# Performance work log

Hardware: AMD Instinct MI355X
Metric: run time of the kernel (lower is better)

## Reference

```python
import jax, jax.numpy as jnp
import numpy as np

B, S1, S2, H1, H2, HID = 8, 512, 512, 128, 128, 128

def setup_inputs() -> dict:
    key = jax.random.key(0)
    ks = jax.random.split(key, 8)
    return {
        "query": jax.random.normal(ks[0], (B, S1, H1), jnp.float32),
        "key": jax.random.normal(ks[1], (B, S2, H2), jnp.float32),
        "value": jax.random.normal(ks[2], (B, S2, H2), jnp.float32),
        "q_mask": jax.random.randint(ks[3], (B, S1), 0, 2, jnp.int32),
        "k_mask": jax.random.randint(ks[4], (B, S2), 0, 2, jnp.int32),
        # init_weights: Linear weight ~ N(0, 0.01), bias = 0
        "W1": jax.random.normal(ks[5], (HID, H1 + H2), jnp.float32) * 0.01,
        "b1": jnp.zeros((HID,), jnp.float32),
        "W2": jax.random.normal(ks[6], (1, HID), jnp.float32) * 0.01,
        "b2": jnp.zeros((1,), jnp.float32),
    }

def reference(query, key, value, q_mask, k_mask, W1, b1, W2, b2):
    h1 = query.shape[-1]
    # Linear on concat([q,k]) == q @ W1[:, :h1].T + k @ W1[:, h1:].T + b1
    qp = jnp.einsum('bsd,hd->bsh', query, W1[:, :h1]) + b1   # [B,S1,HID]
    kp = jnp.einsum('btd,hd->bth', key, W1[:, h1:])          # [B,S2,HID]
    h = jax.nn.relu(qp[:, :, None, :] + kp[:, None, :, :])   # [B,S1,S2,HID]
    s = jnp.einsum('bsth,h->bst', h, W2[0]) + b2[0]          # [B,S1,S2]
    mask = (q_mask[:, :, None] * k_mask[:, None, :]) > 0     # [B,S1,S2]
    A = jnp.where(mask, jnp.exp(s), 0.0)                     # masked_fill(-inf).exp()
    A_sum = jnp.clip(jnp.sum(A, axis=-1, keepdims=True), 2e-15, None)
    attn = A / A_sum
    return jnp.einsum('bst,btd->bsd', attn, value)           # [B,S1,H2]
```

## Files before the change

### kernel.cpp

```cpp
#include <hip/hip_runtime.h>

#define S 512
#define H 128
#define NROW 4096
#define TI 8

__global__ __launch_bounds__(256) void w1t_kernel(const float* __restrict__ W1,
                                                  float* __restrict__ w1T) {
  __shared__ float t[32][33];
  const int d0 = (blockIdx.x & 7) * 32;
  const int h0 = (blockIdx.x >> 3) * 32;
  const int tx = threadIdx.x & 31, ty = threadIdx.x >> 5;
  #pragma unroll
  for (int r = 0; r < 4; r++)
    t[ty + r * 8][tx] = W1[(h0 + ty + r * 8) * 256 + d0 + tx];
  __syncthreads();
  #pragma unroll
  for (int r = 0; r < 4; r++)
    w1T[(size_t)(d0 + ty + r * 8) * H + h0 + tx] = t[tx][ty + r * 8];
}

__global__ __launch_bounds__(256) void proj_kernel(
    const float* __restrict__ query, const float* __restrict__ key,
    const float* __restrict__ w1T, const float* __restrict__ b1,
    const float* __restrict__ W2, const float* __restrict__ b2,
    float* __restrict__ qp, float* __restrict__ kp2,
    float* __restrict__ qw, float* __restrict__ kw)
{
  const int bid = blockIdx.x;
  const bool isq = bid < 256;
  const float* __restrict__ src = isq ? query : key;
  const int rbase = (isq ? bid : bid - 256) * 16;
  const int doff = isq ? 0 : 128;
  const int tid = threadIdx.x;
  const int w = __builtin_amdgcn_readfirstlane(tid >> 6);
  const int lane = tid & 63;
  const int r0w = rbase + w * 4;

  float acc[4][2];
  float2 bv = make_float2(0.f, 0.f);
  if (isq) bv = *(const float2*)(b1 + 2 * lane);
  #pragma unroll
  for (int r = 0; r < 4; r++) { acc[r][0] = bv.x; acc[r][1] = bv.y; }

  for (int dc = 0; dc < 128; dc += 8) {
    float qs[4][8];
    #pragma unroll
    for (int r = 0; r < 4; r++) {
      const float* sp = src + (size_t)(r0w + r) * H + dc;
      #pragma unroll
      for (int u = 0; u < 8; u++) qs[r][u] = sp[u];
    }
    #pragma unroll
    for (int dd = 0; dd < 8; dd++) {
      const float2 wv =
          *(const float2*)(w1T + (size_t)(doff + dc + dd) * H + 2 * lane);
      #pragma unroll
      for (int r = 0; r < 4; r++) {
        acc[r][0] = __builtin_fmaf(qs[r][dd], wv.x, acc[r][0]);
        acc[r][1] = __builtin_fmaf(qs[r][dd], wv.y, acc[r][1]);
      }
    }
  }

  const float2 w2p = *(const float2*)(W2 + 2 * lane);
  const float b2v = b2[0];
  #pragma unroll
  for (int r = 0; r < 4; r++) {
    float t = acc[r][0] * w2p.x + acc[r][1] * w2p.y;
    #pragma unroll
    for (int m = 1; m <= 32; m <<= 1) t += __shfl_xor(t, m, 64);
    if (lane == 0) {
      if (isq) qw[r0w + r] = 0.5f * t + b2v;
      else     kw[r0w + r] = 0.5f * t;
    }
  }

  if (isq) {
    #pragma unroll
    for (int r = 0; r < 4; r++)
      *(float2*)(qp + (size_t)(r0w + r) * H + 2 * lane) =
          make_float2(acc[r][0], acc[r][1]);
  } else {
    #pragma unroll
    for (int r = 0; r < 4; r++)
      *(float2*)(kp2 + ((size_t)(lane >> 3) * NROW + (r0w + r)) * 16 +
                 (lane & 7) * 2) = make_float2(acc[r][0], acc[r][1]);
  }
}

__global__ __launch_bounds__(512) void attn_kernel(
    const float* __restrict__ qp, const float* __restrict__ kp2,
    const float* __restrict__ qw, const float* __restrict__ kw,
    const float* __restrict__ value, const int* __restrict__ q_mask,
    const int* __restrict__ k_mask, const float* __restrict__ W2,
    float* __restrict__ out)
{
  __shared__ float aT[8][64][8];
  __shared__ float numw[8][TI][132];
  __shared__ float denw[8][TI];

  const int it = blockIdx.x;
  const int r0 = it * TI;
  const int b  = r0 >> 9;
  const int tid = threadIdx.x;
  const int w = __builtin_amdgcn_readfirstlane(tid >> 6);
  const int lane = tid & 63;
  const int jg = (b << 9) + (w << 6) + lane;
  const int km = k_mask[jg];
  const float kwj = kw[jg];

  float s[TI];
  #pragma unroll
  for (int i = 0; i < TI; i++) s[i] = 0.f;

  #pragma unroll
  for (int hb = 0; hb < 8; hb++) {
    const float* __restrict__ kptr = kp2 + (((size_t)hb * NROW + jg) << 4);
    const float4 k0 = ((const float4*)kptr)[0];
    const float4 k1 = ((const float4*)kptr)[1];
    const float4 k2 = ((const float4*)kptr)[2];
    const float4 k3 = ((const float4*)kptr)[3];
    const float4* __restrict__ w2c = (const float4*)(W2 + hb * 16);
    const float4 w0 = w2c[0], w1 = w2c[1], w2_ = w2c[2], w3 = w2c[3];
    #pragma unroll
    for (int i = 0; i < TI; i++) {
      const float4* __restrict__ qptr =
          (const float4*)(qp + (size_t)(r0 + i) * H + hb * 16);
      const float4 q0 = qptr[0], q1 = qptr[1], q2 = qptr[2], q3 = qptr[3];
      float t, si = s[i];
      t = q0.x + k0.x; si = __builtin_fmaf(fabsf(t), w0.x, si);
      t = q0.y + k0.y; si = __builtin_fmaf(fabsf(t), w0.y, si);
      t = q0.z + k0.z; si = __builtin_fmaf(fabsf(t), w0.z, si);
      t = q0.w + k0.w; si = __builtin_fmaf(fabsf(t), w0.w, si);
      t = q1.x + k1.x; si = __builtin_fmaf(fabsf(t), w1.x, si);
      t = q1.y + k1.y; si = __builtin_fmaf(fabsf(t), w1.y, si);
      t = q1.z + k1.z; si = __builtin_fmaf(fabsf(t), w1.z, si);
      t = q1.w + k1.w; si = __builtin_fmaf(fabsf(t), w1.w, si);
      t = q2.x + k2.x; si = __builtin_fmaf(fabsf(t), w2_.x, si);
      t = q2.y + k2.y; si = __builtin_fmaf(fabsf(t), w2_.y, si);
      t = q2.z + k2.z; si = __builtin_fmaf(fabsf(t), w2_.z, si);
      t = q2.w + k2.w; si = __builtin_fmaf(fabsf(t), w2_.w, si);
      t = q3.x + k3.x; si = __builtin_fmaf(fabsf(t), w3.x, si);
      t = q3.y + k3.y; si = __builtin_fmaf(fabsf(t), w3.y, si);
      t = q3.z + k3.z; si = __builtin_fmaf(fabsf(t), w3.z, si);
      t = q3.w + k3.w; si = __builtin_fmaf(fabsf(t), w3.w, si);
      s[i] = si;
    }
  }

  float a[TI];
  #pragma unroll
  for (int i = 0; i < TI; i++) {
    const float qws = qw[r0 + i];
    const int qm = q_mask[r0 + i];
    a[i] = (km > 0 && qm > 0) ? __expf(__builtin_fmaf(0.5f, s[i], qws + kwj))
                              : 0.f;
  }
  #pragma unroll
  for (int i = 0; i < TI; i += 2)
    *(float2*)&aT[w][lane][i] = make_float2(a[i], a[i + 1]);
  __syncthreads();

  const int lj = lane >> 5, lh = lane & 31;
  float nr[TI][4];
  float dden[TI];
  #pragma unroll
  for (int i = 0; i < TI; i++) {
    nr[i][0] = 0.f; nr[i][1] = 0.f; nr[i][2] = 0.f; nr[i][3] = 0.f;
    dden[i] = 0.f;
  }
  const float* __restrict__ vbase =
      value + ((size_t)b * S + (w << 6)) * H;

  for (int js = 0; js < 32; js++) {
    const int j = js * 2 + lj;
    const float4 vv = *(const float4*)(vbase + (size_t)j * H + lh * 4);
    const float4 a0 = *(const float4*)&aT[w][j][0];
    const float4 a1 = *(const float4*)&aT[w][j][4];
    const float av[8] = {a0.x, a0.y, a0.z, a0.w, a1.x, a1.y, a1.z, a1.w};
    #pragma unroll
    for (int i = 0; i < TI; i++) {
      nr[i][0] = __builtin_fmaf(av[i], vv.x, nr[i][0]);
      nr[i][1] = __builtin_fmaf(av[i], vv.y, nr[i][1]);
      nr[i][2] = __builtin_fmaf(av[i], vv.z, nr[i][2]);
      nr[i][3] = __builtin_fmaf(av[i], vv.w, nr[i][3]);
      dden[i] += av[i];
    }
  }
  #pragma unroll
  for (int i = 0; i < TI; i++) {
    #pragma unroll
    for (int k = 0; k < 4; k++) nr[i][k] += __shfl_xor(nr[i][k], 32, 64);
    dden[i] += __shfl_xor(dden[i], 32, 64);
  }
  if (lj == 0) {
    #pragma unroll
    for (int i = 0; i < TI; i++)
      *(float4*)&numw[w][i][lh * 4] =
          make_float4(nr[i][0], nr[i][1], nr[i][2], nr[i][3]);
    if (lane == 0) {
      #pragma unroll
      for (int i = 0; i < TI; i++) denw[w][i] = dden[i];
    }
  }
  __syncthreads();

  {
    const int i = w;
    float2 acc = make_float2(0.f, 0.f);
    float den = 0.f;
    #pragma unroll
    for (int ww = 0; ww < 8; ww++) {
      const float2 p = *(const float2*)&numw[ww][i][lane * 2];
      acc.x += p.x; acc.y += p.y;
      den += denw[ww][i];
    }
    const float inv = 1.f / fmaxf(den, 2e-15f);
    *(float2*)(out + (size_t)(r0 + i) * H + lane * 2) =
        make_float2(acc.x * inv, acc.y * inv);
  }
}

extern "C" void kernel_launch(void* const* d_in, const int* in_sizes, int n_in,
                              void* d_out, int out_size, void* d_ws, size_t ws_size,
                              hipStream_t stream)
{
  (void)in_sizes; (void)n_in; (void)out_size; (void)ws_size;
  const float* query  = (const float*)d_in[0];
  const float* key    = (const float*)d_in[1];
  const float* value  = (const float*)d_in[2];
  const int*   q_mask = (const int*)d_in[3];
  const int*   k_mask = (const int*)d_in[4];
  const float* W1     = (const float*)d_in[5];
  const float* b1     = (const float*)d_in[6];
  const float* W2     = (const float*)d_in[7];
  const float* b2     = (const float*)d_in[8];
  float* out = (float*)d_out;

  float* ws   = (float*)d_ws;
  float* w1T  = ws;
  float* qp   = w1T + 256 * H;
  float* kp2  = qp + (size_t)NROW * H;
  float* qw   = kp2 + (size_t)NROW * H;
  float* kw   = qw + NROW;

  w1t_kernel<<<32, 256, 0, stream>>>(W1, w1T);
  proj_kernel<<<512, 256, 0, stream>>>(query, key, w1T, b1, W2, b2,
                                       qp, kp2, qw, kw);
  attn_kernel<<<512, 512, 0, stream>>>(qp, kp2, qw, kw, value, q_mask,
                                       k_mask, W2, out);
}
```

Baseline: 128.6 us.

## Restructure score loop into row pairs with occupancy hint and drop redundant barrier

The attention score phase now walks four 32-wide hidden chunks, keeping key and W2 chunks in registers and processing query rows two at a time in non-unrolled loops. The kernel also gets a minimum-occupancy launch bound of 4 blocks. The barrier after writing the per-wave aT tile is removed, since each wave reads only its own slice. The projection kernel processes 16-wide chunks and preloads the W1 slices before the FMAs. Together these aim to cut register pressure and raise occupancy, at the risk of spills under the tighter register cap and less instruction-level parallelism from the rolled loops.

Measured after the change: 125.0 us. -2.8%, faster.

```diff
diff --git a/kernel.cpp b/kernel.cpp
--- a/kernel.cpp
+++ b/kernel.cpp
@@ -43,22 +43,25 @@
   #pragma unroll
   for (int r = 0; r < 4; r++) { acc[r][0] = bv.x; acc[r][1] = bv.y; }
 
-  for (int dc = 0; dc < 128; dc += 8) {
-    float qs[4][8];
+  #pragma unroll 1
+  for (int dc = 0; dc < 128; dc += 16) {
+    float qs[4][16];
     #pragma unroll
     for (int r = 0; r < 4; r++) {
       const float* sp = src + (size_t)(r0w + r) * H + dc;
       #pragma unroll
-      for (int u = 0; u < 8; u++) qs[r][u] = sp[u];
-    }
-    #pragma unroll
-    for (int dd = 0; dd < 8; dd++) {
-      const float2 wv =
-          *(const float2*)(w1T + (size_t)(doff + dc + dd) * H + 2 * lane);
+      for (int u = 0; u < 16; u++) qs[r][u] = sp[u];
+    }
+    float2 wv[16];
+    #pragma unroll
+    for (int dd = 0; dd < 16; dd++)
+      wv[dd] = *(const float2*)(w1T + (size_t)(doff + dc + dd) * H + 2 * lane);
+    #pragma unroll
+    for (int dd = 0; dd < 16; dd++) {
       #pragma unroll
       for (int r = 0; r < 4; r++) {
-        acc[r][0] = __builtin_fmaf(qs[r][dd], wv.x, acc[r][0]);
-        acc[r][1] = __builtin_fmaf(qs[r][dd], wv.y, acc[r][1]);
+        acc[r][0] = __builtin_fmaf(qs[r][dd], wv[dd].x, acc[r][0]);
+        acc[r][1] = __builtin_fmaf(qs[r][dd], wv[dd].y, acc[r][1]);
       }
     }
   }
@@ -89,7 +92,7 @@
   }
 }
 
-__global__ __launch_bounds__(512) void attn_kernel(
+__global__ __launch_bounds__(512, 4) void attn_kernel(
     const float* __restrict__ qp, const float* __restrict__ kp2,
     const float* __restrict__ qw, const float* __restrict__ kw,
     const float* __restrict__ value, const int* __restrict__ q_mask,
@@ -114,38 +117,40 @@
   #pragma unroll
   for (int i = 0; i < TI; i++) s[i] = 0.f;
 
-  #pragma unroll
-  for (int hb = 0; hb < 8; hb++) {
-    const float* __restrict__ kptr = kp2 + (((size_t)hb * NROW + jg) << 4);
-    const float4 k0 = ((const float4*)kptr)[0];
-    const float4 k1 = ((const float4*)kptr)[1];
-    const float4 k2 = ((const float4*)kptr)[2];
-    const float4 k3 = ((const float4*)kptr)[3];
-    const float4* __restrict__ w2c = (const float4*)(W2 + hb * 16);
-    const float4 w0 = w2c[0], w1 = w2c[1], w2_ = w2c[2], w3 = w2c[3];
-    #pragma unroll
-    for (int i = 0; i < TI; i++) {
-      const float4* __restrict__ qptr =
-          (const float4*)(qp + (size_t)(r0 + i) * H + hb * 16);
-      const float4 q0 = qptr[0], q1 = qptr[1], q2 = qptr[2], q3 = qptr[3];
-      float t, si = s[i];
-      t = q0.x + k0.x; si = __builtin_fmaf(fabsf(t), w0.x, si);
-      t = q0.y + k0.y; si = __builtin_fmaf(fabsf(t), w0.y, si);
-      t = q0.z + k0.z; si = __builtin_fmaf(fabsf(t), w0.z, si);
-      t = q0.w + k0.w; si = __builtin_fmaf(fabsf(t), w0.w, si);
-      t = q1.x + k1.x; si = __builtin_fmaf(fabsf(t), w1.x, si);
-      t = q1.y + k1.y; si = __builtin_fmaf(fabsf(t), w1.y, si);
-      t = q1.z + k1.z; si = __builtin_fmaf(fabsf(t), w1.z, si);
-      t = q1.w + k1.w; si = __builtin_fmaf(fabsf(t), w1.w, si);
-      t = q2.x + k2.x; si = __builtin_fmaf(fabsf(t), w2_.x, si);
-      t = q2.y + k2.y; si = __builtin_fmaf(fabsf(t), w2_.y, si);
-      t = q2.z + k2.z; si = __builtin_fmaf(fabsf(t), w2_.z, si);
-      t = q2.w + k2.w; si = __builtin_fmaf(fabsf(t), w2_.w, si);
-      t = q3.x + k3.x; si = __builtin_fmaf(fabsf(t), w3.x, si);
-      t = q3.y + k3.y; si = __builtin_fmaf(fabsf(t), w3.y, si);
-      t = q3.z + k3.z; si = __builtin_fmaf(fabsf(t), w3.z, si);
-      t = q3.w + k3.w; si = __builtin_fmaf(fabsf(t), w3.w, si);
-      s[i] = si;
+  #pragma unroll 1
+  for (int p = 0; p < 4; p++) {
+    float kr[32];
+    {
+      const float* __restrict__ k0 = kp2 + (((size_t)(2 * p) * NROW + jg) << 4);
+      const float* __restrict__ k1 = kp2 + (((size_t)(2 * p + 1) * NROW + jg) << 4);
+      #pragma unroll
+      for (int u = 0; u < 4; u++) {
+        *(float4*)&kr[u * 4]      = ((const float4*)k0)[u];
+        *(float4*)&kr[16 + u * 4] = ((const float4*)k1)[u];
+      }
+    }
+    float w2r[32];
+    #pragma unroll
+    for (int u = 0; u < 8; u++)
+      *(float4*)&w2r[u * 4] = ((const float4*)(W2 + p * 32))[u];
+
+    #pragma unroll 1
+    for (int ip = 0; ip < TI; ip += 2) {
+      float q0[32], q1[32];
+      {
+        const float* __restrict__ qa = qp + (size_t)(r0 + ip) * H + p * 32;
+        #pragma unroll
+        for (int u = 0; u < 32; u++) { q0[u] = qa[u]; q1[u] = qa[H + u]; }
+      }
+      float s0 = s[ip], s1 = s[ip + 1];
+      #pragma unroll
+      for (int u = 0; u < 32; u++) {
+        const float t0 = q0[u] + kr[u];
+        const float t1 = q1[u] + kr[u];
+        s0 = __builtin_fmaf(fabsf(t0), w2r[u], s0);
+        s1 = __builtin_fmaf(fabsf(t1), w2r[u], s1);
+      }
+      s[ip] = s0; s[ip + 1] = s1;
     }
   }
 
@@ -158,9 +163,8 @@
                               : 0.f;
   }
   #pragma unroll
-  for (int i = 0; i < TI; i += 2)
-    *(float2*)&aT[w][lane][i] = make_float2(a[i], a[i + 1]);
-  __syncthreads();
+  for (int i = 0; i < TI; i += 4)
+    *(float4*)&aT[w][lane][i] = make_float4(a[i], a[i+1], a[i+2], a[i+3]);
 
   const int lj = lane >> 5, lh = lane & 31;
   float nr[TI][4];
@@ -173,6 +177,7 @@
   const float* __restrict__ vbase =
       value + ((size_t)b * S + (w << 6)) * H;
 
+  #pragma unroll 1
   for (int js = 0; js < 32; js++) {
     const int j = js * 2 + lj;
     const float4 vv = *(const float4*)(vbase + (size_t)j * H + lh * 4);
```
